# Kernel tuning notes

Measured on AMD Instinct MI355X. Metric: run time of the kernel, lower is better.

The kernel has to match this reference:

```python
import jax, jax.numpy as jnp
import numpy as np

N = 1_000_000
D = 128
S = 16384


def setup_inputs() -> dict:
    key = jax.random.key(0)
    k_x, k_idx, k_w, k_b = jax.random.split(key, 4)
    x = jax.random.normal(k_x, (N, D), dtype=jnp.float32)
    index = jnp.sort(jax.random.randint(k_idx, (N,), 0, S, dtype=jnp.int64))
    # single plain Linear layer of PyG MLP([D, D], plain_last=True)
    lim = 1.0 / np.sqrt(D)
    W = jax.random.uniform(k_w, (D, D), dtype=jnp.float32, minval=-lim, maxval=lim)
    b = jax.random.uniform(k_b, (D,), dtype=jnp.float32, minval=-lim, maxval=lim)
    return {"x": x, "W": W, "b": b, "index": index, "num_segments": S}


def reference(x, W, b, index, num_segments):
    # att = MLP(x): single plain linear layer (no activation, plain_last=True)
    att = x @ W.T + b  # [N, D]
    # segment softmax over nodes within each graph, per channel (PyG softmax)
    seg_max = jax.ops.segment_max(att, index, num_segments=num_segments)  # [S, D]
    e = jnp.exp(att - seg_max[index])  # [N, D]
    seg_sum = jax.ops.segment_sum(e, index, num_segments=num_segments)  # [S, D]
    att = e / (seg_sum[index] + 1e-16)  # [N, D]
    # attention-weighted global add pool
    return jax.ops.segment_sum(x * att, index, num_segments=num_segments)  # [S, D]
```

## Files before the change

### kernel.cpp

```cpp
#include <hip/hip_runtime.h>
#include <hip/hip_bf16.h>

#define SEGS   16384
#define DCH    128
#define CHUNK  32
#define SEGPB  4
#define XHBLK  520
#define LOG2E  1.4426950408889634f

using f32x4  = __attribute__((ext_vector_type(4))) float;
using bf16x8 = __attribute__((ext_vector_type(8))) short;
using u32x2  = __attribute__((ext_vector_type(2))) unsigned int;
using u32x4  = __attribute__((ext_vector_type(4))) unsigned int;

__device__ __forceinline__ float u2f(unsigned int u) { return __uint_as_float(u); }
__device__ __forceinline__ unsigned int f2u(float f) { return __float_as_uint(f); }

__global__ void setup_kernel(const float* __restrict__ W,
                             const int* __restrict__ index, int N,
                             unsigned short* __restrict__ WfH,
                             int* __restrict__ seg_start) {
  int i = blockIdx.x * blockDim.x + threadIdx.x;
  if (i < DCH * DCH) {
    int n = i >> 7, k = i & 127;
    float w = W[i] * LOG2E;
    unsigned int u = f2u(w);
    unsigned int r = (u + 0x7FFFu + ((u >> 16) & 1)) >> 16;
    int kt    = k >> 5;
    int ntile = n >> 4;
    int lane  = (n & 15) + 16 * ((k >> 3) & 3);
    int j     = k & 7;
    int dst = ((kt * 8 + ntile) * 64 + lane) * 8 + j;
    WfH[dst] = (unsigned short)r;
  } else if (i < DCH * DCH + SEGS + 1) {
    int s = i - DCH * DCH;
    int lo = 0, hi = N;
    while (lo < hi) {
      int mid = (lo + hi) >> 1;
      if (index[mid] < s) lo = mid + 1; else hi = mid;
    }
    seg_start[s] = lo;
  }
}

__global__ __launch_bounds__(256) void pool_kernel(
    const float* __restrict__ x, const float* __restrict__ bias,
    const int* __restrict__ seg_start,
    const u32x4* __restrict__ WfH,
    float* __restrict__ out) {
  __shared__ unsigned short xh[2][8 * XHBLK];

  const int t    = threadIdx.x;
  const int wv   = t >> 6;
  const int lane = t & 63;
  const int cl   = lane & 15;
  const int g    = lane >> 4;
  const int k31  = t & 31;
  const int lrow = t >> 5;
  const int lcol = k31 << 2;

  const int xh_base   = 1040 * (k31 >> 3) + 8 * lrow + 128 * ((k31 >> 1) & 3) + 4 * (k31 & 1);
  const int frag_base = lane * 8;
  const int exd = wv * 520 + 16 * g + 64 * (cl >> 3) + ((cl & 7) >> 1);
  const int shl = (cl & 1) ? 0 : 16;

  u32x4 bh[4][2];
#pragma unroll
  for (int kt = 0; kt < 4; ++kt)
#pragma unroll
    for (int nt = 0; nt < 2; ++nt) {
      int off = (kt * 8 + (wv * 2 + nt)) * 64 + lane;
      bh[kt][nt] = WfH[off];
    }

  const float bc0 = bias[wv * 32 + cl]      * LOG2E;
  const float bc1 = bias[wv * 32 + 16 + cl] * LOG2E;

  const int s0   = blockIdx.x * SEGPB;
  const int sEnd = s0 + SEGPB;
  const int R0   = seg_start[s0];
  const int R1   = seg_start[sEnd];

  if (R0 == R1) {
    if (lane < 16) {
      for (int es = s0; es < sEnd; ++es) {
        out[(size_t)es * DCH + wv * 32 + cl]      = 0.f;
        out[(size_t)es * DCH + wv * 32 + 16 + cl] = 0.f;
      }
    }
    return;
  }

  int curSeg = s0;
  int segEnd = seg_start[curSeg + 1];
  int c0 = R0;

  f32x4 pv[4];
#pragma unroll
  for (int p = 0; p < 4; ++p) {
    int lr = c0 + lrow + p * 8;
    f32x4 v = {0.f, 0.f, 0.f, 0.f};
    if (lr < R1) v = *(const f32x4*)(x + (size_t)lr * DCH + lcol);
    pv[p] = v;
  }

  float den[2] = {0.f, 0.f};
  float num[2] = {0.f, 0.f};

  auto body = [&](unsigned short* XH) -> bool {
    const unsigned int* XHd = (const unsigned int*)XH;

#pragma unroll
    for (int p = 0; p < 4; ++p) {
      f32x4 v = pv[p];
      unsigned int u0 = f2u(v[0]) + 0x8000u, u1 = f2u(v[1]) + 0x8000u;
      unsigned int u2 = f2u(v[2]) + 0x8000u, u3 = f2u(v[3]) + 0x8000u;
      u32x2 H = { (u1 & 0xFFFF0000u) | (u0 >> 16),
                  (u3 & 0xFFFF0000u) | (u2 >> 16) };
      *(u32x2*)&XH[xh_base + (p >> 1) * XHBLK + (p & 1) * 64] = H;
    }

    const int nc0 = c0 + CHUNK;
    if (nc0 < R1) {
#pragma unroll
      for (int p = 0; p < 4; ++p) {
        int lr = nc0 + lrow + p * 8;
        f32x4 v = {0.f, 0.f, 0.f, 0.f};
        if (lr < R1) v = *(const f32x4*)(x + (size_t)lr * DCH + lcol);
        pv[p] = v;
      }
    }

    asm volatile("s_waitcnt lgkmcnt(0)" ::: "memory");
    __builtin_amdgcn_sched_barrier(0);
    __builtin_amdgcn_s_barrier();
    __builtin_amdgcn_sched_barrier(0);

    f32x4 Cf[2][2];
#pragma unroll
    for (int mt = 0; mt < 2; ++mt) {
      Cf[mt][0] = (f32x4){bc0, bc0, bc0, bc0};
      Cf[mt][1] = (f32x4){bc1, bc1, bc1, bc1};
    }
#pragma unroll
    for (int kt = 0; kt < 4; ++kt) {
      u32x4 ah[2];
#pragma unroll
      for (int mt = 0; mt < 2; ++mt)
        ah[mt] = *(const u32x4*)&XH[frag_base + (2 * kt + mt) * XHBLK];
#pragma unroll
      for (int mt = 0; mt < 2; ++mt)
#pragma unroll
        for (int nt = 0; nt < 2; ++nt) {
          bf16x8 A = __builtin_bit_cast(bf16x8, ah[mt]);
          bf16x8 B = __builtin_bit_cast(bf16x8, bh[kt][nt]);
          Cf[mt][nt] = __builtin_amdgcn_mfma_f32_16x16x32_bf16(A, B, Cf[mt][nt], 0, 0, 0);
        }
    }

    float pr[2][2][4], xv[2][2][4];
#pragma unroll
    for (int nt = 0; nt < 2; ++nt)
#pragma unroll
      for (int mt = 0; mt < 2; ++mt)
#pragma unroll
        for (int r = 0; r < 4; ++r) {
          pr[nt][mt][r] = __builtin_amdgcn_exp2f(Cf[mt][nt][r]);
          unsigned int xu = XHd[exd + mt * 260 + nt * 128 + r * 4];
          xv[nt][mt][r] = u2f((xu << shl) & 0xFFFF0000u);
        }

    const int lim = c0 + CHUNK;
    int lo = c0;
    while (curSeg < sEnd) {
      const int hi  = segEnd;
      const int hiC = (hi < lim) ? hi : lim;
      const unsigned span = (unsigned)(hiC - lo);
#pragma unroll
      for (int nt = 0; nt < 2; ++nt)
#pragma unroll
        for (int mt = 0; mt < 2; ++mt)
#pragma unroll
          for (int r = 0; r < 4; ++r) {
            const int row = c0 + mt * 16 + g * 4 + r;
            const bool use = (unsigned)(row - lo) < span;
            const float pp = use ? pr[nt][mt][r] : 0.f;
            den[nt] += pp;
            num[nt] += pp * xv[nt][mt][r];
          }
      if (hi <= lim) {
#pragma unroll
        for (int nt = 0; nt < 2; ++nt) {
          float l = den[nt], a = num[nt];
          l += __shfl_xor(l, 16); l += __shfl_xor(l, 32);
          a += __shfl_xor(a, 16); a += __shfl_xor(a, 32);
          if (lane < 16)
            out[(size_t)curSeg * DCH + wv * 32 + nt * 16 + cl] = a / (l + 1e-16f);
          den[nt] = 0.f; num[nt] = 0.f;
        }
        lo = hi;
        ++curSeg;
        if (curSeg < sEnd) segEnd = seg_start[curSeg + 1];
      } else {
        break;
      }
    }
    if (curSeg >= sEnd) return false;
    c0 = nc0;
    return true;
  };

  for (;;) {
    if (!body(&xh[0][0])) break;
    if (!body(&xh[1][0])) break;
  }
}

extern "C" void kernel_launch(void* const* d_in, const int* in_sizes, int n_in,
                              void* d_out, int out_size, void* d_ws, size_t ws_size,
                              hipStream_t stream) {
  const float* x    = (const float*)d_in[0];
  const float* W    = (const float*)d_in[1];
  const float* bias = (const float*)d_in[2];
  const int*   idx  = (const int*)d_in[3];
  const int N = in_sizes[0] / DCH;

  unsigned short* WfH = (unsigned short*)d_ws;
  int* seg = (int*)(WfH + DCH * DCH);

  int setup_threads = DCH * DCH + SEGS + 1;
  setup_kernel<<<(setup_threads + 255) / 256, 256, 0, stream>>>(W, idx, N, WfH, seg);
  pool_kernel<<<SEGS / SEGPB, 256, 0, stream>>>(x, bias, seg,
                                                (const u32x4*)WfH,
                                                (float*)d_out);
}
```

Measured before the change: 116.9 us.

## Use 512-thread blocks with 64-row chunks, one 16-column tile per wave

```diff
diff --git a/kernel.cpp b/kernel.cpp
--- a/kernel.cpp
+++ b/kernel.cpp
@@ -3,8 +3,8 @@
 
 #define SEGS   16384
 #define DCH    128
-#define CHUNK  32
-#define SEGPB  4
+#define CHUNK  64
+#define SEGPB  8
 #define XHBLK  520
 #define LOG2E  1.4426950408889634f
 
@@ -43,12 +43,12 @@
   }
 }
 
-__global__ __launch_bounds__(256) void pool_kernel(
+__global__ __launch_bounds__(512) void pool_kernel(
     const float* __restrict__ x, const float* __restrict__ bias,
     const int* __restrict__ seg_start,
     const u32x4* __restrict__ WfH,
     float* __restrict__ out) {
-  __shared__ unsigned short xh[2][8 * XHBLK];
+  __shared__ unsigned short xh[2][16 * XHBLK];
 
   const int t    = threadIdx.x;
   const int wv   = t >> 6;
@@ -59,22 +59,19 @@
   const int lrow = t >> 5;
   const int lcol = k31 << 2;
 
-  const int xh_base   = 1040 * (k31 >> 3) + 8 * lrow + 128 * ((k31 >> 1) & 3) + 4 * (k31 & 1);
+  const int xh_base   = (k31 >> 3) * (4 * XHBLK) + 8 * lrow
+                      + 128 * ((k31 >> 1) & 3) + 4 * (k31 & 1);
   const int frag_base = lane * 8;
-  const int exd = wv * 520 + 16 * g + 64 * (cl >> 3) + ((cl & 7) >> 1);
+  const int exd = 4 * (wv >> 1) * 260 + 16 * g
+                + 64 * (2 * (wv & 1) + (cl >> 3)) + ((cl & 7) >> 1);
   const int shl = (cl & 1) ? 0 : 16;
 
-  u32x4 bh[4][2];
+  u32x4 bh[4];
 #pragma unroll
   for (int kt = 0; kt < 4; ++kt)
-#pragma unroll
-    for (int nt = 0; nt < 2; ++nt) {
-      int off = (kt * 8 + (wv * 2 + nt)) * 64 + lane;
-      bh[kt][nt] = WfH[off];
-    }
-
-  const float bc0 = bias[wv * 32 + cl]      * LOG2E;
-  const float bc1 = bias[wv * 32 + 16 + cl] * LOG2E;
+    bh[kt] = WfH[(kt * 8 + wv) * 64 + lane];
+
+  const float bc = bias[wv * 16 + cl] * LOG2E;
 
   const int s0   = blockIdx.x * SEGPB;
   const int sEnd = s0 + SEGPB;
@@ -83,10 +80,8 @@
 
   if (R0 == R1) {
     if (lane < 16) {
-      for (int es = s0; es < sEnd; ++es) {
-        out[(size_t)es * DCH + wv * 32 + cl]      = 0.f;
-        out[(size_t)es * DCH + wv * 32 + 16 + cl] = 0.f;
-      }
+      for (int es = s0; es < sEnd; ++es)
+        out[(size_t)es * DCH + wv * 16 + cl] = 0.f;
     }
     return;
   }
@@ -98,14 +93,13 @@
   f32x4 pv[4];
 #pragma unroll
   for (int p = 0; p < 4; ++p) {
-    int lr = c0 + lrow + p * 8;
+    int lr = c0 + lrow + p * 16;
     f32x4 v = {0.f, 0.f, 0.f, 0.f};
     if (lr < R1) v = *(const f32x4*)(x + (size_t)lr * DCH + lcol);
     pv[p] = v;
   }
 
-  float den[2] = {0.f, 0.f};
-  float num[2] = {0.f, 0.f};
+  float den = 0.f, num = 0.f;
 
   auto body = [&](unsigned short* XH) -> bool {
     const unsigned int* XHd = (const unsigned int*)XH;
@@ -117,14 +111,14 @@
       unsigned int u2 = f2u(v[2]) + 0x8000u, u3 = f2u(v[3]) + 0x8000u;
       u32x2 H = { (u1 & 0xFFFF0000u) | (u0 >> 16),
                   (u3 & 0xFFFF0000u) | (u2 >> 16) };
-      *(u32x2*)&XH[xh_base + (p >> 1) * XHBLK + (p & 1) * 64] = H;
+      *(u32x2*)&XH[xh_base + p * XHBLK] = H;
     }
 
     const int nc0 = c0 + CHUNK;
     if (nc0 < R1) {
 #pragma unroll
       for (int p = 0; p < 4; ++p) {
-        int lr = nc0 + lrow + p * 8;
+        int lr = nc0 + lrow + p * 16;
         f32x4 v = {0.f, 0.f, 0.f, 0.f};
         if (lr < R1) v = *(const f32x4*)(x + (size_t)lr * DCH + lcol);
         pv[p] = v;
@@ -136,39 +130,37 @@
     __builtin_amdgcn_s_barrier();
     __builtin_amdgcn_sched_barrier(0);
 
-    f32x4 Cf[2][2];
-#pragma unroll
-    for (int mt = 0; mt < 2; ++mt) {
-      Cf[mt][0] = (f32x4){bc0, bc0, bc0, bc0};
-      Cf[mt][1] = (f32x4){bc1, bc1, bc1, bc1};
-    }
+    f32x4 Cf[4];
+#pragma unroll
+    for (int mt = 0; mt < 4; ++mt)
+      Cf[mt] = (f32x4){bc, bc, bc, bc};
 #pragma unroll
     for (int kt = 0; kt < 4; ++kt) {
-      u32x4 ah[2];
-#pragma unroll
-      for (int mt = 0; mt < 2; ++mt)
-        ah[mt] = *(const u32x4*)&XH[frag_base + (2 * kt + mt) * XHBLK];
-#pragma unroll
-      for (int mt = 0; mt < 2; ++mt)
-#pragma unroll
-        for (int nt = 0; nt < 2; ++nt) {
-          bf16x8 A = __builtin_bit_cast(bf16x8, ah[mt]);
-          bf16x8 B = __builtin_bit_cast(bf16x8, bh[kt][nt]);
-          Cf[mt][nt] = __builtin_amdgcn_mfma_f32_16x16x32_bf16(A, B, Cf[mt][nt], 0, 0, 0);
-        }
-    }
-
-    float pr[2][2][4], xv[2][2][4];
-#pragma unroll
-    for (int nt = 0; nt < 2; ++nt)
-#pragma unroll
-      for (int mt = 0; mt < 2; ++mt)
-#pragma unroll
-        for (int r = 0; r < 4; ++r) {
-          pr[nt][mt][r] = __builtin_amdgcn_exp2f(Cf[mt][nt][r]);
-          unsigned int xu = XHd[exd + mt * 260 + nt * 128 + r * 4];
-          xv[nt][mt][r] = u2f((xu << shl) & 0xFFFF0000u);
-        }
+      u32x4 ah[4];
+#pragma unroll
+      for (int mt = 0; mt < 4; ++mt)
+        ah[mt] = *(const u32x4*)&XH[frag_base + (4 * kt + mt) * XHBLK];
+#pragma unroll
+      for (int mt = 0; mt < 4; ++mt) {
+        bf16x8 A = __builtin_bit_cast(bf16x8, ah[mt]);
+        bf16x8 B = __builtin_bit_cast(bf16x8, bh[kt]);
+        Cf[mt] = __builtin_amdgcn_mfma_f32_16x16x32_bf16(A, B, Cf[mt], 0, 0, 0);
+      }
+    }
+
+    float xv[4][4], pr[4][4];
+#pragma unroll
+    for (int mt = 0; mt < 4; ++mt)
+#pragma unroll
+      for (int r = 0; r < 4; ++r) {
+        unsigned int xu = XHd[exd + mt * 260 + r * 4];
+        xv[mt][r] = u2f((xu << shl) & 0xFFFF0000u);
+      }
+#pragma unroll
+    for (int mt = 0; mt < 4; ++mt)
+#pragma unroll
+      for (int r = 0; r < 4; ++r)
+        pr[mt][r] = __builtin_amdgcn_exp2f(Cf[mt][r]);
 
     const int lim = c0 + CHUNK;
     int lo = c0;
@@ -177,27 +169,22 @@
       const int hiC = (hi < lim) ? hi : lim;
       const unsigned span = (unsigned)(hiC - lo);
 #pragma unroll
-      for (int nt = 0; nt < 2; ++nt)
-#pragma unroll
-        for (int mt = 0; mt < 2; ++mt)
-#pragma unroll
-          for (int r = 0; r < 4; ++r) {
-            const int row = c0 + mt * 16 + g * 4 + r;
-            const bool use = (unsigned)(row - lo) < span;
-            const float pp = use ? pr[nt][mt][r] : 0.f;
-            den[nt] += pp;
-            num[nt] += pp * xv[nt][mt][r];
-          }
+      for (int mt = 0; mt < 4; ++mt)
+#pragma unroll
+        for (int r = 0; r < 4; ++r) {
+          const int row = c0 + mt * 16 + g * 4 + r;
+          const bool use = (unsigned)(row - lo) < span;
+          const float pp = use ? pr[mt][r] : 0.f;
+          den += pp;
+          num += pp * xv[mt][r];
+        }
       if (hi <= lim) {
-#pragma unroll
-        for (int nt = 0; nt < 2; ++nt) {
-          float l = den[nt], a = num[nt];
-          l += __shfl_xor(l, 16); l += __shfl_xor(l, 32);
-          a += __shfl_xor(a, 16); a += __shfl_xor(a, 32);
-          if (lane < 16)
-            out[(size_t)curSeg * DCH + wv * 32 + nt * 16 + cl] = a / (l + 1e-16f);
-          den[nt] = 0.f; num[nt] = 0.f;
-        }
+        float l = den, a = num;
+        l += __shfl_xor(l, 16); l += __shfl_xor(l, 32);
+        a += __shfl_xor(a, 16); a += __shfl_xor(a, 32);
+        if (lane < 16)
+          out[(size_t)curSeg * DCH + wv * 16 + cl] = a / (l + 1e-16f);
+        den = 0.f; num = 0.f;
         lo = hi;
         ++curSeg;
         if (curSeg < sEnd) segEnd = seg_start[curSeg + 1];
@@ -230,7 +217,7 @@
 
   int setup_threads = DCH * DCH + SEGS + 1;
   setup_kernel<<<(setup_threads + 255) / 256, 256, 0, stream>>>(W, idx, N, WfH, seg);
-  pool_kernel<<<SEGS / SEGPB, 256, 0, stream>>>(x, bias, seg,
+  pool_kernel<<<SEGS / SEGPB, 512, 0, stream>>>(x, bias, seg,
                                                 (const u32x4*)WfH,
                                                 (float*)d_out);
 }
```

Result: slower. 161.1 us (+37.7%).
